# Optimization experiments

Measured on AMD Instinct MI355X. Metric: run time of the kernel, lower is better.

The kernel has to match this reference:

```python
import jax, jax.numpy as jnp
import numpy as np

D = 256        # embedding_dim
N = 32768      # number of latent vectors (tokens)
K = 8192       # num_embeddings (codebook size)


def setup_inputs() -> dict:
    key = jax.random.key(0)
    k1, k2 = jax.random.split(key)
    z_e = jax.random.normal(k1, (D, N), dtype=jnp.float32)
    embeddings = jax.random.normal(k2, (K, D), dtype=jnp.float32)
    return {"z_e": z_e, "embeddings": embeddings}


def reference(z_e, embeddings):
    # z_e: (D, N), embeddings: (K, D)
    z = z_e.T  # (N, D)
    # squared euclidean distance via expansion ||z||^2 - 2 z.e + ||e||^2
    # (mathematically identical to sum((emb - z)**2, -1), avoids (N,K,D) temp)
    z_sq = jnp.sum(z * z, axis=1, keepdims=True)            # (N, 1)
    e_sq = jnp.sum(embeddings * embeddings, axis=1)         # (K,)
    dist = z_sq - 2.0 * (z @ embeddings.T) + e_sq[None, :]  # (N, K)
    indices = jnp.argmin(dist, axis=-1)                     # (N,)
    z_q = embeddings[indices].T                             # (D, N)
    return z_q, indices
```

## Files before the change

### kernel.cpp

```cpp
#include <hip/hip_runtime.h>

#define D_DIM 256
#define N_TOK 32768
#define K_CB  8192
#define TAU   0.12f
#define ZC_CAP 4096
#define SLABS 32
#define SLABW 256

typedef float    f32x16 __attribute__((ext_vector_type(16)));
typedef float    f32x4  __attribute__((ext_vector_type(4)));
typedef _Float16 f16x8  __attribute__((ext_vector_type(8)));

#define OFF_ESQ   0
#define OFF_CNT   32768
#define OFF_GDONE 33024
#define OFF_LIST  35072
#define OFF_FIXB  166144
#define OFF_EHT   524288
#define OFF_ZC    (OFF_EHT + 4194304)
#define MAXGRP    512
#define WS_NEED   ((size_t)(OFF_ZC + 4194304))

#define SMEM_MAIN 65536

__global__ __launch_bounds__(256) void eprep_kernel(const float* __restrict__ e,
                                                    short* __restrict__ eht,
                                                    float* __restrict__ esq,
                                                    int* __restrict__ cnt,
                                                    int* __restrict__ gdone) {
  __shared__ float ps[4 * 64];
  const int tid = threadIdx.x;
  const int kk = tid & 63, cc = tid >> 6;
  const int k = blockIdx.x * 64 + kk;
  if (blockIdx.x == 0) {
    if (tid == 0) *cnt = 0;
    if (tid < 256) { gdone[tid] = 0; gdone[tid + 256] = 0; }
  }
  _Float16* ef = (_Float16*)eht;
  float ss = 0.f;
  #pragma unroll
  for (int c2 = 0; c2 < 8; ++c2) {
    const int c = cc * 8 + c2;
    f32x4 v0 = *(const f32x4*)(e + (size_t)k * D_DIM + c * 8);
    f32x4 v1 = *(const f32x4*)(e + (size_t)k * D_DIM + c * 8 + 4);
    float v[8] = {v0[0], v0[1], v0[2], v0[3], v1[0], v1[1], v1[2], v1[3]};
    f16x8 hv;
    #pragma unroll
    for (int i = 0; i < 8; ++i) {
      ss += v[i] * v[i];
      hv[i] = (_Float16)v[i];
    }
    *(f16x8*)(ef + ((size_t)c * K_CB + k) * 8) = hv;
  }
  ps[cc * 64 + kk] = ss;
  __syncthreads();
  if (tid < 64)
    esq[blockIdx.x * 64 + tid] = ps[tid] + ps[64 + tid] + ps[128 + tid] + ps[192 + tid];
}

__global__ __launch_bounds__(1024, 4) void vq_main_kernel(
    const float* __restrict__ z, const float* __restrict__ e,
    const float* __restrict__ esq_g,
    const short* __restrict__ eht,
    float* __restrict__ out,
    int* __restrict__ cnt, int* __restrict__ list,
    unsigned long long* __restrict__ fixb, float* __restrict__ zc) {
  extern __shared__ char smem[];
  _Float16* zs = (_Float16*)smem;
  __shared__ int fin[128], slo[128];

  const int tid  = threadIdx.x;
  const int w    = tid >> 6;
  const int lane = tid & 63;
  const int half = lane >> 5;
  const int l31  = lane & 31;
  const int n0   = blockIdx.x * 128;
  const _Float16* ef = (const _Float16*)eht;

  {
    const int t  = tid & 127;
    const int cb = (tid >> 7) * 4;
    #pragma unroll
    for (int cc = 0; cc < 4; ++cc) {
      const int c = cb + cc;
      f16x8 hv;
      #pragma unroll
      for (int i = 0; i < 8; ++i)
        hv[i] = (_Float16)(-2.0f * z[(size_t)(c * 8 + i) * N_TOK + n0 + t]);
      *(f16x8*)(zs + ((size_t)c * 128 + t) * 8) = hv;
    }
  }
  __syncthreads();

  float bestv[4] = {3.4e38f, 3.4e38f, 3.4e38f, 3.4e38f};
  float secv[4]  = {3.4e38f, 3.4e38f, 3.4e38f, 3.4e38f};
  int   bestk[4] = {0, 0, 0, 0};

  for (int k0 = 0; k0 < K_CB; k0 += 512) {
    const int kb = k0 + w * 32;

    f32x16 acc[4];
    {
      const int qb = kb + 4 * half;
      #pragma unroll
      for (int g = 0; g < 4; ++g) {
        f32x4 q = *(const f32x4*)(esq_g + qb + 8 * g);
        #pragma unroll
        for (int r = 0; r < 4; ++r) {
          const float qv = q[r];
          #pragma unroll
          for (int j = 0; j < 4; ++j) acc[j][g * 4 + r] = qv;
        }
      }
    }

    #pragma unroll 2
    for (int dc = 0; dc < 16; ++dc) {
      f16x8 a, b[4];
      a = *(const f16x8*)(ef + ((size_t)(2 * dc + half) * K_CB + kb + l31) * 8);
      const int zb = ((2 * dc + half) * 128 + l31) * 8;
      #pragma unroll
      for (int j = 0; j < 4; ++j)
        b[j] = *(const f16x8*)(zs + zb + j * 32 * 8);
      #pragma unroll
      for (int j = 0; j < 4; ++j)
        acc[j] = __builtin_amdgcn_mfma_f32_32x32x16_f16(a, b[j], acc[j], 0, 0, 0);
    }

    {
      const int base = kb + 4 * half;
      #pragma unroll
      for (int g = 0; g < 4; ++g) {
        #pragma unroll
        for (int r = 0; r < 4; ++r) {
          const int reg = g * 4 + r;
          const int kglob = base + 8 * g + r;
          #pragma unroll
          for (int j = 0; j < 4; ++j) {
            const float s = acc[j][reg];
            if (s < bestv[j]) { secv[j] = bestv[j]; bestv[j] = s; bestk[j] = kglob; }
            else if (s < secv[j]) secv[j] = s;
          }
        }
      }
    }
  }

  __syncthreads();
  float* pv  = (float*)(smem);
  int*   pk  = (int*)  (smem + 16384);
  float* ps2 = (float*)(smem + 32768);
  const int slot = w * 2 + half;
  #pragma unroll
  for (int j = 0; j < 4; ++j) {
    const int t = j * 32 + l31;
    pv [slot * 128 + t] = bestv[j];
    pk [slot * 128 + t] = bestk[j];
    ps2[slot * 128 + t] = secv[j];
  }
  __syncthreads();
  if (tid < 128) {
    const int t = tid;
    float bv = pv[t]; int bk = pk[t]; float sc = ps2[t];
    #pragma unroll
    for (int s2 = 1; s2 < 32; ++s2) {
      float v = pv[s2 * 128 + t]; int k2 = pk[s2 * 128 + t]; float s3 = ps2[s2 * 128 + t];
      if (v < bv || (v == bv && k2 < bk)) { sc = fminf(bv, s3); bv = v; bk = k2; }
      else                                { sc = fminf(sc, v); }
    }
    fin[t] = bk;
    int sl = -1;
    const int n = n0 + t;
    out[(size_t)D_DIM * N_TOK + n] = (float)bk;
    if (sc - bv < TAU) {
      int p = atomicAdd(cnt, 1);
      list[p] = n;
      fixb[n] = 0xFFFFFFFFFFFFFFFFULL;
      if (p < ZC_CAP) sl = p;
    }
    slo[t] = sl;
  }
  __syncthreads();

  for (int tt = 0; tt < 128; ++tt) {
    const int p = slo[tt];
    if (p >= 0 && tid < 256)
      zc[(size_t)p * 256 + tid] = z[(size_t)tid * N_TOK + n0 + tt];
  }

  {
    const int t = tid & 127, d0 = tid >> 7;
    const int kk = fin[t];
    const f32x4* row = (const f32x4*)(e + (size_t)kk * D_DIM) + d0 * 8;
    #pragma unroll 4
    for (int q = 0; q < 8; ++q) {
      f32x4 v = row[q];
      const int d = d0 * 32 + q * 4;
      out[(size_t)(d + 0) * N_TOK + n0 + t] = v[0];
      out[(size_t)(d + 1) * N_TOK + n0 + t] = v[1];
      out[(size_t)(d + 2) * N_TOK + n0 + t] = v[2];
      out[(size_t)(d + 3) * N_TOK + n0 + t] = v[3];
    }
  }
}

__global__ __launch_bounds__(256) void rescan_kernel(
    const float* __restrict__ z, const float* __restrict__ zc,
    const float* __restrict__ e,
    const float* __restrict__ esq, const int* __restrict__ cnt,
    const int* __restrict__ list, unsigned long long* __restrict__ fixb,
    int* __restrict__ gdone, float* __restrict__ out) {
  __shared__ float zs[D_DIM * 64];
  __shared__ unsigned long long red[16 * 64];
  __shared__ int fk[64], fn[64], lastflag;
  const int tid = threadIdx.x;
  const int c = *(volatile const int*)cnt;
  if (c == 0) return;
  int groups = (c + 63) >> 6;
  if (groups > MAXGRP) groups = MAXGRP;
  const int items = groups * SLABS;
  const int tx = tid & 15, ty = tid >> 4;

  for (int it = blockIdx.x; it < items; it += gridDim.x) {
    const int g = it / SLABS;
    const int slab = (it % SLABS) * SLABW;
    __syncthreads();
    if (g < (ZC_CAP >> 6)) {
      const int t = tid & 63, seg = tid >> 6;
      const int idx = g * 64 + t;
      const float* src = zc + (size_t)(idx < c ? idx : c - 1) * 256 + seg * 64;
      #pragma unroll
      for (int r = 0; r < 16; ++r) {
        f32x4 v = *(const f32x4*)(src + r * 4);
        const int d = seg * 64 + r * 4;
        zs[(d + 0) * 64 + t] = v[0];
        zs[(d + 1) * 64 + t] = v[1];
        zs[(d + 2) * 64 + t] = v[2];
        zs[(d + 3) * 64 + t] = v[3];
      }
    } else {
      const int t = tid & 63, dq = tid >> 6;
      const int idx = g * 64 + t;
      const int n = list[idx < c ? idx : c - 1];
      #pragma unroll 4
      for (int dd = 0; dd < 64; ++dd) {
        const int d = dq * 64 + dd;
        zs[d * 64 + t] = z[(size_t)d * N_TOK + n];
      }
    }
    __syncthreads();

    unsigned long long lmin[4] = {~0ULL, ~0ULL, ~0ULL, ~0ULL};
    #pragma unroll
    for (int k0 = 0; k0 < SLABW; k0 += 64) {
      const f32x4* er[4]; float eqv[4];
      #pragma unroll
      for (int j = 0; j < 4; ++j) {
        int k = slab + k0 + ty + 16 * j;
        er[j] = (const f32x4*)(e + (size_t)k * D_DIM);
        eqv[j] = esq[k];
      }
      float acc[4][4];
      #pragma unroll
      for (int i = 0; i < 4; ++i)
        #pragma unroll
        for (int j = 0; j < 4; ++j) acc[i][j] = 0.f;
      #pragma unroll 4
      for (int d4 = 0; d4 < D_DIM / 4; ++d4) {
        f32x4 ev[4];
        #pragma unroll
        for (int j = 0; j < 4; ++j) ev[j] = er[j][d4];
        #pragma unroll
        for (int dd = 0; dd < 4; ++dd) {
          float zv[4];
          #pragma unroll
          for (int i = 0; i < 4; ++i) zv[i] = zs[(d4 * 4 + dd) * 64 + tx + 16 * i];
          #pragma unroll
          for (int i = 0; i < 4; ++i)
            #pragma unroll
            for (int j = 0; j < 4; ++j) acc[i][j] += zv[i] * ev[j][dd];
        }
      }
      #pragma unroll
      for (int j = 0; j < 4; ++j) {
        const int k = slab + k0 + ty + 16 * j;
        #pragma unroll
        for (int i = 0; i < 4; ++i) {
          float s = eqv[j] - 2.0f * acc[i][j] + 1024.0f;
          unsigned long long p =
              ((unsigned long long)__float_as_uint(s) << 32) | (unsigned)k;
          lmin[i] = (p < lmin[i]) ? p : lmin[i];
        }
      }
    }
    #pragma unroll
    for (int i = 0; i < 4; ++i) red[ty * 64 + tx + 16 * i] = lmin[i];
    __syncthreads();
    if (tid < 64) {
      unsigned long long m = red[tid];
      #pragma unroll
      for (int t = 1; t < 16; ++t) {
        unsigned long long v = red[t * 64 + tid];
        m = (v < m) ? v : m;
      }
      const int idx = g * 64 + tid;
      const int n = list[idx < c ? idx : c - 1];
      atomicMin(&fixb[n], m);
    }
    __threadfence();
    __syncthreads();
    if (tid == 0) lastflag = (atomicAdd(&gdone[g], 1) == SLABS - 1) ? 1 : 0;
    __syncthreads();
    if (lastflag) {
      if (tid < 64) {
        const int idx = g * 64 + tid;
        int kres = -1, n = -1;
        if (idx < c) {
          n = list[idx];
          unsigned long long mv = atomicMin(&fixb[n], 0xFFFFFFFFFFFFFFFFULL);
          kres = (int)(unsigned)(mv & 0xFFFFFFFFu);
          out[(size_t)D_DIM * N_TOK + n] = (float)kres;
        }
        fk[tid] = kres; fn[tid] = n;
      }
      __syncthreads();
      {
        const int t = tid & 63, dq = tid >> 6;
        const int kres = fk[t];
        if (kres >= 0) {
          const int n = fn[t];
          const float* row = e + (size_t)kres * D_DIM;
          #pragma unroll 4
          for (int dd = 0; dd < 64; ++dd) {
            const int d = dq * 64 + dd;
            out[(size_t)d * N_TOK + n] = row[d];
          }
        }
      }
    }
  }
}

__global__ __launch_bounds__(256) void esq_kernel(const float* __restrict__ e,
                                                  float* __restrict__ esq) {
  const int wave = threadIdx.x >> 6, lane = threadIdx.x & 63;
  const int k = blockIdx.x * 4 + wave;
  const float4* row = (const float4*)(e + (size_t)k * D_DIM);
  float4 v = row[lane];
  float s = v.x*v.x + v.y*v.y + v.z*v.z + v.w*v.w;
  #pragma unroll
  for (int off = 32; off > 0; off >>= 1) s += __shfl_down(s, off, 64);
  if (lane == 0) esq[k] = s;
}

__global__ __launch_bounds__(256) void vq_kernel(const float* __restrict__ z,
                                                 const float* __restrict__ e,
                                                 const float* __restrict__ esq,
                                                 float* __restrict__ out) {
  __shared__ float zs[D_DIM][64];
  const int tid = threadIdx.x, tx = tid & 15, ty = tid >> 4;
  const int n0 = blockIdx.x * 64;
  {
    const int c = tid & 63, d0 = tid >> 6;
    #pragma unroll 4
    for (int d = d0; d < D_DIM; d += 4) zs[d][c] = z[(size_t)d * N_TOK + n0 + c];
  }
  __syncthreads();
  float bestv[4] = {3.4e38f,3.4e38f,3.4e38f,3.4e38f};
  int   besti[4] = {0,0,0,0};
  for (int k0 = 0; k0 < K_CB; k0 += 64) {
    const float4* er[4]; float eqv[4];
    #pragma unroll
    for (int j = 0; j < 4; ++j) {
      int k = k0 + ty + 16 * j;
      er[j] = (const float4*)(e + (size_t)k * D_DIM);
      eqv[j] = esq[k];
    }
    float acc[4][4];
    #pragma unroll
    for (int i = 0; i < 4; ++i)
      #pragma unroll
      for (int j = 0; j < 4; ++j) acc[i][j] = 0.f;
    #pragma unroll 4
    for (int d4 = 0; d4 < D_DIM/4; ++d4) {
      float4 ev[4];
      #pragma unroll
      for (int j = 0; j < 4; ++j) ev[j] = er[j][d4];
      #pragma unroll
      for (int dd = 0; dd < 4; ++dd) {
        float zv[4];
        #pragma unroll
        for (int i = 0; i < 4; ++i) zv[i] = zs[d4*4+dd][tx + 16*i];
        #pragma unroll
        for (int i = 0; i < 4; ++i)
          #pragma unroll
          for (int j = 0; j < 4; ++j) acc[i][j] += zv[i] * ((const float*)&ev[j])[dd];
      }
    }
    #pragma unroll
    for (int j = 0; j < 4; ++j) {
      int k = k0 + ty + 16 * j;
      #pragma unroll
      for (int i = 0; i < 4; ++i) {
        float s = eqv[j] - 2.0f * acc[i][j];
        if (s < bestv[i]) { bestv[i] = s; besti[i] = k; }
      }
    }
  }
  __syncthreads();
  float* lds = &zs[0][0];
  float* vred = lds; int* ired = (int*)lds + 1024; int* fin = (int*)lds + 2048;
  #pragma unroll
  for (int i = 0; i < 4; ++i) {
    int l = tx + 16 * i;
    vred[ty * 64 + l] = bestv[i]; ired[ty * 64 + l] = besti[i];
  }
  __syncthreads();
  if (tid < 64) {
    float bv = vred[tid]; int bi = ired[tid];
    #pragma unroll
    for (int t = 1; t < 16; ++t) {
      float v = vred[t*64+tid]; int ix = ired[t*64+tid];
      if (v < bv || (v == bv && ix < bi)) { bv = v; bi = ix; }
    }
    fin[tid] = bi;
    out[(size_t)D_DIM * N_TOK + n0 + tid] = (float)bi;
  }
  __syncthreads();
  {
    const int l = tid & 63, d0 = tid >> 6;
    const int kk = fin[l];
    const float* row = e + (size_t)kk * D_DIM;
    #pragma unroll 4
    for (int d = d0; d < D_DIM; d += 4) out[(size_t)d * N_TOK + n0 + l] = row[d];
  }
}

extern "C" void kernel_launch(void* const* d_in, const int* in_sizes, int n_in,
                              void* d_out, int out_size, void* d_ws, size_t ws_size,
                              hipStream_t stream) {
  const float* z = (const float*)d_in[0];
  const float* e = (const float*)d_in[1];
  float* out = (float*)d_out;
  char* ws = (char*)d_ws;

  if (ws_size >= WS_NEED) {
    float* esq = (float*)(ws + OFF_ESQ);
    int* cnt = (int*)(ws + OFF_CNT);
    int* gdone = (int*)(ws + OFF_GDONE);
    int* list = (int*)(ws + OFF_LIST);
    unsigned long long* fixb = (unsigned long long*)(ws + OFF_FIXB);
    short* eht = (short*)(ws + OFF_EHT);
    float* zc = (float*)(ws + OFF_ZC);

    (void)hipFuncSetAttribute((const void*)vq_main_kernel,
                              hipFuncAttributeMaxDynamicSharedMemorySize, SMEM_MAIN);

    eprep_kernel<<<128, 256, 0, stream>>>(e, eht, esq, cnt, gdone);
    vq_main_kernel<<<256, 1024, SMEM_MAIN, stream>>>(z, e, esq, eht,
                                                     out, cnt, list, fixb, zc);
    rescan_kernel<<<512, 256, 0, stream>>>(z, zc, e, esq, cnt, list, fixb, gdone, out);
  } else {
    float* esq = (float*)(ws);
    esq_kernel<<<K_CB / 4, 256, 0, stream>>>(e, esq);
    vq_kernel<<<N_TOK / 64, 256, 0, stream>>>(z, e, esq, out);
  }
}
```

Before: 340.5 us.

## Retile MFMA warp work to 2x2 codebook-by-token fragments

Each of the 16 waves now covers 64 codebook entries by 64 tokens as a 2x2 grid of 32x32 MFMA tiles, instead of 32 codebook entries by all 128 tokens. This halves the per-wave LDS token-fragment loads per MFMA and balances global codebook loads against shared loads. The price is twice the global eht traffic per wave. The final cross-wave reduction now merges 16 partial slots instead of 32, with the shared scratch layout adjusted to match.

```diff
diff --git a/kernel.cpp b/kernel.cpp
--- a/kernel.cpp
+++ b/kernel.cpp
@@ -75,6 +75,8 @@
   const int lane = tid & 63;
   const int half = lane >> 5;
   const int l31  = lane & 31;
+  const int th   = w >> 3;
+  const int cg   = w & 7;
   const int n0   = blockIdx.x * 128;
   const _Float16* ef = (const _Float16*)eht;
 
@@ -93,43 +95,48 @@
   }
   __syncthreads();
 
-  float bestv[4] = {3.4e38f, 3.4e38f, 3.4e38f, 3.4e38f};
-  float secv[4]  = {3.4e38f, 3.4e38f, 3.4e38f, 3.4e38f};
-  int   bestk[4] = {0, 0, 0, 0};
+  float bestv[2] = {3.4e38f, 3.4e38f};
+  float secv[2]  = {3.4e38f, 3.4e38f};
+  int   bestk[2] = {0, 0};
 
   for (int k0 = 0; k0 < K_CB; k0 += 512) {
-    const int kb = k0 + w * 32;
-
-    f32x16 acc[4];
-    {
-      const int qb = kb + 4 * half;
+    const int kb = k0 + cg * 64;
+
+    f32x16 acc[2][2];
+    #pragma unroll
+    for (int f = 0; f < 2; ++f) {
+      const int qb = kb + 32 * f + 4 * half;
       #pragma unroll
       for (int g = 0; g < 4; ++g) {
         f32x4 q = *(const f32x4*)(esq_g + qb + 8 * g);
         #pragma unroll
         for (int r = 0; r < 4; ++r) {
           const float qv = q[r];
-          #pragma unroll
-          for (int j = 0; j < 4; ++j) acc[j][g * 4 + r] = qv;
+          acc[f][0][g * 4 + r] = qv;
+          acc[f][1][g * 4 + r] = qv;
         }
       }
     }
 
     #pragma unroll 2
     for (int dc = 0; dc < 16; ++dc) {
-      f16x8 a, b[4];
-      a = *(const f16x8*)(ef + ((size_t)(2 * dc + half) * K_CB + kb + l31) * 8);
-      const int zb = ((2 * dc + half) * 128 + l31) * 8;
-      #pragma unroll
-      for (int j = 0; j < 4; ++j)
-        b[j] = *(const f16x8*)(zs + zb + j * 32 * 8);
-      #pragma unroll
-      for (int j = 0; j < 4; ++j)
-        acc[j] = __builtin_amdgcn_mfma_f32_32x32x16_f16(a, b[j], acc[j], 0, 0, 0);
-    }
-
-    {
-      const int base = kb + 4 * half;
+      f16x8 a[2], b[2];
+      const size_t ebase = ((size_t)(2 * dc + half) * K_CB + kb + l31) * 8;
+      a[0] = *(const f16x8*)(ef + ebase);
+      a[1] = *(const f16x8*)(ef + ebase + 32 * 8);
+      const int zb = ((2 * dc + half) * 128 + th * 64 + l31) * 8;
+      b[0] = *(const f16x8*)(zs + zb);
+      b[1] = *(const f16x8*)(zs + zb + 32 * 8);
+      #pragma unroll
+      for (int f = 0; f < 2; ++f)
+        #pragma unroll
+        for (int j = 0; j < 2; ++j)
+          acc[f][j] = __builtin_amdgcn_mfma_f32_32x32x16_f16(a[f], b[j], acc[f][j], 0, 0, 0);
+    }
+
+    #pragma unroll
+    for (int f = 0; f < 2; ++f) {
+      const int base = kb + 32 * f + 4 * half;
       #pragma unroll
       for (int g = 0; g < 4; ++g) {
         #pragma unroll
@@ -137,8 +144,8 @@
           const int reg = g * 4 + r;
           const int kglob = base + 8 * g + r;
           #pragma unroll
-          for (int j = 0; j < 4; ++j) {
-            const float s = acc[j][reg];
+          for (int j = 0; j < 2; ++j) {
+            const float s = acc[f][j][reg];
             if (s < bestv[j]) { secv[j] = bestv[j]; bestv[j] = s; bestk[j] = kglob; }
             else if (s < secv[j]) secv[j] = s;
           }
@@ -149,12 +156,12 @@
 
   __syncthreads();
   float* pv  = (float*)(smem);
-  int*   pk  = (int*)  (smem + 16384);
-  float* ps2 = (float*)(smem + 32768);
-  const int slot = w * 2 + half;
+  int*   pk  = (int*)  (smem + 8192);
+  float* ps2 = (float*)(smem + 16384);
+  const int slot = cg * 2 + half;
   #pragma unroll
-  for (int j = 0; j < 4; ++j) {
-    const int t = j * 32 + l31;
+  for (int j = 0; j < 2; ++j) {
+    const int t = th * 64 + j * 32 + l31;
     pv [slot * 128 + t] = bestv[j];
     pk [slot * 128 + t] = bestk[j];
     ps2[slot * 128 + t] = secv[j];
@@ -164,7 +171,7 @@
     const int t = tid;
     float bv = pv[t]; int bk = pk[t]; float sc = ps2[t];
     #pragma unroll
-    for (int s2 = 1; s2 < 32; ++s2) {
+    for (int s2 = 1; s2 < 16; ++s2) {
       float v = pv[s2 * 128 + t]; int k2 = pk[s2 * 128 + t]; float s3 = ps2[s2 * 128 + t];
       if (v < bv || (v == bv && k2 < bk)) { sc = fminf(bv, s3); bv = v; bk = k2; }
       else                                { sc = fminf(sc, v); }
```

Result: no change. 342.4 us (+0.6%).
